# Performance work log

Measured on AMD Instinct MI355X. Metric: run time of the kernel, lower is better.

## Reference

```python
import jax, jax.numpy as jnp
import numpy as np

N_NODES = 100000
N_EDGES = 3200000
F_IN = 256
D_OUT = 64
BATCH = 4096
N_FIELDS = 20


def setup_inputs() -> dict:
    key = jax.random.key(0)
    k1, k2, k3, k4 = jax.random.split(key, 4)
    features = jax.random.normal(k1, (N_NODES, F_IN), dtype=jnp.float32)
    edge_index = jax.random.randint(k2, (2, N_EDGES), 0, N_NODES, dtype=jnp.int32)
    W = jax.random.normal(k3, (F_IN, D_OUT), dtype=jnp.float32) * 0.05
    b = jnp.zeros((D_OUT,), dtype=jnp.float32)
    x = jax.random.randint(k4, (BATCH, N_FIELDS), 0, N_NODES, dtype=jnp.int32)
    return {"features": features, "edge_index": edge_index, "W": W, "b": b, "x": x}


def reference(features, edge_index, W, b, x):
    # PyG GCNConv: add self-loops, symmetric normalization, linear transform,
    # scatter-add aggregation, then final index by x.
    n = features.shape[0]
    loop = jnp.arange(n, dtype=edge_index.dtype)
    src = jnp.concatenate([edge_index[0], loop])  # [E+N]
    dst = jnp.concatenate([edge_index[1], loop])
    ones = jnp.ones(src.shape[0], dtype=features.dtype)
    deg = jax.ops.segment_sum(ones, dst, num_segments=n)  # in-degree incl. self-loop
    deg_inv_sqrt = jnp.where(deg > 0, jax.lax.rsqrt(deg), 0.0)
    norm = deg_inv_sqrt[src] * deg_inv_sqrt[dst]  # [E+N]
    xw = features @ W  # [N, D] -- transform before aggregation (fewer FLOPs)
    msg = xw[src] * norm[:, None]  # gather + scale
    out = jax.ops.segment_sum(msg, dst, num_segments=n) + b  # [N, D]
    return out[x]  # [batch, num_fields, D]
```

## Files before the change

### kernel.cpp

```cpp
#include <hip/hip_runtime.h>
#include <hip/hip_bf16.h>

#define N_NODES 100000
#define N_EDGES 3200000
#define F_IN 256
#define D_OUT 64
#define BATCH 4096
#define N_FIELDS 20
#define N_ENTRIES (BATCH * N_FIELDS)

#define NBUCKET 512
#define NPB 196
#define N_PAD (NBUCKET * NPB)
#define EPB 8192
#define NBLK ((N_EDGES + EPB - 1) / EPB)
#define BUCKET_CAP 8192
#define SCAN_B 512
#define NSB (N_PAD / SCAN_B)

typedef short bf16x8 __attribute__((ext_vector_type(8)));
typedef float f32x4 __attribute__((ext_vector_type(4)));

static __device__ __forceinline__ float bfbits2f(unsigned short u) {
    return __uint_as_float((unsigned)u << 16);
}
static __device__ __forceinline__ unsigned short f2bf_bits(float x) {
    __hip_bfloat16 h = __float2bfloat16(x);
    return *reinterpret_cast<unsigned short*>(&h);
}

__global__ __launch_bounds__(256) void k_hist(const uint4* __restrict__ dst4,
                                              unsigned short* __restrict__ perBlockCnt) {
    __shared__ unsigned hist[NBUCKET];
    hist[threadIdx.x] = 0;
    hist[threadIdx.x + 256] = 0;
    __syncthreads();
    int base4 = blockIdx.x * (EPB / 4);
#pragma unroll
    for (int k = 0; k < EPB / 1024; k++) {
        int e4 = base4 + k * 256 + threadIdx.x;
        if (e4 < N_EDGES / 4) {
            uint4 d = dst4[e4];
            atomicAdd(&hist[d.x / NPB], 1u);
            atomicAdd(&hist[d.y / NPB], 1u);
            atomicAdd(&hist[d.z / NPB], 1u);
            atomicAdd(&hist[d.w / NPB], 1u);
        }
    }
    __syncthreads();
    perBlockCnt[(threadIdx.x) * NBLK + blockIdx.x] = (unsigned short)hist[threadIdx.x];
    perBlockCnt[(threadIdx.x + 256) * NBLK + blockIdx.x] = (unsigned short)hist[threadIdx.x + 256];
}

__global__ __launch_bounds__(256) void k_colscan_w(unsigned short* __restrict__ perBlockCnt,
                                                   int* __restrict__ bucketTot) {
    int gw = (blockIdx.x * 256 + threadIdx.x) >> 6;
    int lane = threadIdx.x & 63;
    if (gw >= NBUCKET) return;
    unsigned running = 0;
    for (int c = 0; c < (NBLK + 63) / 64; c++) {
        int blk = c * 64 + lane;
        int idx = gw * NBLK + blk;
        unsigned v = (blk < NBLK) ? perBlockCnt[idx] : 0;
        unsigned orig = v;
#pragma unroll
        for (int d = 1; d < 64; d <<= 1) {
            unsigned t = __shfl_up(v, d, 64);
            if (lane >= d) v += t;
        }
        if (blk < NBLK) perBlockCnt[idx] = (unsigned short)(running + v - orig);
        running += __shfl(v, 63, 64);
    }
    if (lane == 0) bucketTot[gw] = (int)running;
}

__global__ __launch_bounds__(512) void k_basescan(const int* __restrict__ bucketTot,
                                                  int* __restrict__ bucketBase) {
    __shared__ int sh[NBUCKET];
    int tid = threadIdx.x;
    int v = bucketTot[tid];
    sh[tid] = v;
    __syncthreads();
    for (int off = 1; off < NBUCKET; off <<= 1) {
        int t = (tid >= off) ? sh[tid - off] : 0;
        __syncthreads();
        sh[tid] += t;
        __syncthreads();
    }
    bucketBase[tid] = sh[tid] - v;
    if (tid == NBUCKET - 1) bucketBase[NBUCKET] = sh[NBUCKET - 1];
}

__global__ __launch_bounds__(256) void k_bucket_scatter(const uint4* __restrict__ src4,
                                                        const uint4* __restrict__ dst4,
                                                        const int* __restrict__ bucketBase,
                                                        const unsigned short* __restrict__ perBlockCnt,
                                                        unsigned* __restrict__ bucketData) {
    __shared__ unsigned slotBase[NBUCKET];
    slotBase[threadIdx.x] = (unsigned)bucketBase[threadIdx.x] +
                            (unsigned)perBlockCnt[threadIdx.x * NBLK + blockIdx.x];
    slotBase[threadIdx.x + 256] = (unsigned)bucketBase[threadIdx.x + 256] +
                                  (unsigned)perBlockCnt[(threadIdx.x + 256) * NBLK + blockIdx.x];
    __syncthreads();
    int base4 = blockIdx.x * (EPB / 4);
#pragma unroll
    for (int k = 0; k < EPB / 1024; k++) {
        int e4 = base4 + k * 256 + threadIdx.x;
        if (e4 < N_EDGES / 4) {
            uint4 s = src4[e4];
            uint4 d = dst4[e4];
            unsigned ss[4] = {s.x, s.y, s.z, s.w};
            unsigned dd[4] = {d.x, d.y, d.z, d.w};
#pragma unroll
            for (int j = 0; j < 4; j++) {
                unsigned b = dd[j] / NPB;
                unsigned ld = dd[j] - b * NPB;
                unsigned slot = atomicAdd(&slotBase[b], 1u);
                bucketData[slot] = ss[j] | (ld << 17);
            }
        }
    }
}

__global__ __launch_bounds__(256) void kx_cnt(const int* __restrict__ x,
                                              int* __restrict__ nodeEntCnt,
                                              unsigned* __restrict__ refBits) {
    int ent = blockIdx.x * blockDim.x + threadIdx.x;
    if (ent < N_ENTRIES) {
        int node = x[ent];
        atomicAdd(&nodeEntCnt[node], 1);
        atomicOr(&refBits[node >> 5], 1u << (node & 31));
    }
}

__global__ __launch_bounds__(512) void kx_scan_local(const int* __restrict__ nodeEntCnt,
                                                     int* __restrict__ localE,
                                                     int* __restrict__ blockSumsE) {
    __shared__ int sh[SCAN_B];
    int g = blockIdx.x * SCAN_B + threadIdx.x;
    int v = (g < N_PAD) ? nodeEntCnt[g] : 0;
    sh[threadIdx.x] = v;
    __syncthreads();
    for (int off = 1; off < SCAN_B; off <<= 1) {
        int t = (threadIdx.x >= off) ? sh[threadIdx.x - off] : 0;
        __syncthreads();
        sh[threadIdx.x] += t;
        __syncthreads();
    }
    int incl = sh[threadIdx.x];
    if (g < N_PAD) localE[g] = incl - v;
    if (threadIdx.x == SCAN_B - 1) blockSumsE[blockIdx.x] = incl;
}

__global__ void kx_scan_blocks(const int* __restrict__ blockSumsE,
                               int* __restrict__ blockBaseE) {
    if (threadIdx.x == 0 && blockIdx.x == 0) {
        int s = 0;
        for (int i = 0; i < NSB; i++) {
            blockBaseE[i] = s;
            s += blockSumsE[i];
        }
    }
}

__global__ __launch_bounds__(256) void kx_scatter(const int* __restrict__ x,
                                                  int* __restrict__ localE,
                                                  const int* __restrict__ blockBaseE,
                                                  int* __restrict__ entGrouped) {
    int ent = blockIdx.x * blockDim.x + threadIdx.x;
    if (ent < N_ENTRIES) {
        int node = x[ent];
        int posL = atomicAdd(&localE[node], 1);
        entGrouped[blockBaseE[node >> 9] + posL] = ent;
    }
}

__global__ __launch_bounds__(256) void k_bucket_csr(unsigned* __restrict__ bucketData,
                                                    const int* __restrict__ bucketBase,
                                                    const unsigned* __restrict__ refBits,
                                                    int* __restrict__ rowStart,
                                                    unsigned short* __restrict__ deg) {
    __shared__ unsigned words[BUCKET_CAP];
    __shared__ unsigned srcsorted[BUCKET_CAP];
    __shared__ unsigned nodeCount[NPB];
    __shared__ unsigned sscan[256];
    __shared__ unsigned cursor[NPB];
    __shared__ unsigned char refF[NPB];

    int b = blockIdx.x;
    int base = bucketBase[b];
    int cnt = bucketBase[b + 1] - base;
    if (cnt > BUCKET_CAP) cnt = BUCKET_CAP;
    int tid = threadIdx.x;

    for (int j = tid; j < NPB; j += 256) nodeCount[j] = 0;
    __syncthreads();

    for (int i = tid; i < cnt; i += 256) {
        unsigned w = bucketData[base + i];
        words[i] = w;
        atomicAdd(&nodeCount[w >> 17], 1u);
    }
    __syncthreads();

    int firstNode = b * NPB;
    unsigned refCnt = 0;
    if (tid < NPB) {
        int node = firstNode + tid;
        unsigned isRef = (refBits[node >> 5] >> (node & 31)) & 1u;
        refF[tid] = (unsigned char)isRef;
        refCnt = isRef ? nodeCount[tid] : 0;
        deg[node] = (unsigned short)nodeCount[tid];
    }
    sscan[tid] = refCnt;
    __syncthreads();
    for (int off = 1; off < 256; off <<= 1) {
        unsigned t = (tid >= off) ? sscan[tid - off] : 0;
        __syncthreads();
        sscan[tid] += t;
        __syncthreads();
    }

    if (tid < NPB) {
        unsigned excl = sscan[tid] - refCnt;
        rowStart[firstNode + tid] = base + (int)excl;
        cursor[tid] = excl;
    }
    __syncthreads();

    for (int i = tid; i < cnt; i += 256) {
        unsigned w = words[i];
        unsigned ld = w >> 17;
        if (refF[ld]) {
            unsigned slot = atomicAdd(&cursor[ld], 1u);
            srcsorted[slot] = w & 0x1FFFFu;
        }
    }
    __syncthreads();

    int refTotal = (int)sscan[255];
    for (int i = tid; i < refTotal; i += 256)
        bucketData[base + i] = srcsorted[i];
}

__global__ void k_wtconv(const float* __restrict__ W, unsigned short* __restrict__ WTbf) {
    int i = blockIdx.x * blockDim.x + threadIdx.x;
    if (i >= D_OUT * F_IN) return;
    int n = i >> 8, k = i & 255;
    WTbf[i] = f2bf_bits(W[k * D_OUT + n]);
}

__global__ __launch_bounds__(256) void k_gemm_mfma(const float* __restrict__ feat,
                                                   const unsigned short* __restrict__ WTbf,
                                                   const unsigned short* __restrict__ deg,
                                                   unsigned short* __restrict__ y) {
    __shared__ unsigned short wt[64 * 264];
    int tid = threadIdx.x;
    {
        int r = tid >> 2, seg = tid & 3;
        const uint4* gsrc = (const uint4*)(WTbf + r * 256 + seg * 64);
        uint4* ldst = (uint4*)&wt[r * 264 + seg * 64];
#pragma unroll
        for (int q = 0; q < 8; q++) ldst[q] = gsrc[q];
    }
    __syncthreads();

    int wave = tid >> 6, lane = tid & 63;
    int quad = lane >> 4, m = lane & 15;
    int rowT = blockIdx.x * 64 + wave * 16;
    int row = rowT + m;
    int rowC = (row < N_NODES) ? row : (N_NODES - 1);
    const float* fb = feat + (size_t)rowC * F_IN + quad * 8;

    f32x4 acc0 = {0.f, 0.f, 0.f, 0.f};
    f32x4 acc1 = acc0, acc2 = acc0, acc3 = acc0;

#pragma unroll
    for (int kk = 0; kk < 8; kk++) {
        float4 x0 = *(const float4*)(fb + kk * 32);
        float4 x1 = *(const float4*)(fb + kk * 32 + 4);
        bf16x8 a;
        a[0] = (short)f2bf_bits(x0.x); a[1] = (short)f2bf_bits(x0.y);
        a[2] = (short)f2bf_bits(x0.z); a[3] = (short)f2bf_bits(x0.w);
        a[4] = (short)f2bf_bits(x1.x); a[5] = (short)f2bf_bits(x1.y);
        a[6] = (short)f2bf_bits(x1.z); a[7] = (short)f2bf_bits(x1.w);
        int kbase = kk * 32 + quad * 8;
        bf16x8 b0 = *(const bf16x8*)&wt[(0 * 16 + m) * 264 + kbase];
        bf16x8 b1 = *(const bf16x8*)&wt[(1 * 16 + m) * 264 + kbase];
        bf16x8 b2 = *(const bf16x8*)&wt[(2 * 16 + m) * 264 + kbase];
        bf16x8 b3 = *(const bf16x8*)&wt[(3 * 16 + m) * 264 + kbase];
        acc0 = __builtin_amdgcn_mfma_f32_16x16x32_bf16(a, b0, acc0, 0, 0, 0);
        acc1 = __builtin_amdgcn_mfma_f32_16x16x32_bf16(a, b1, acc1, 0, 0, 0);
        acc2 = __builtin_amdgcn_mfma_f32_16x16x32_bf16(a, b2, acc2, 0, 0, 0);
        acc3 = __builtin_amdgcn_mfma_f32_16x16x32_bf16(a, b3, acc3, 0, 0, 0);
    }

    float dv[4];
#pragma unroll
    for (int r = 0; r < 4; r++) {
        int rr = rowT + quad * 4 + r;
        dv[r] = rsqrtf((float)(deg[rr] + 1));
    }
#pragma unroll
    for (int r = 0; r < 4; r++) {
        int rr = rowT + quad * 4 + r;
        if (rr < N_NODES) {
            size_t o = (size_t)rr * D_OUT + m;
            y[o]      = f2bf_bits(acc0[r] * dv[r]);
            y[o + 16] = f2bf_bits(acc1[r] * dv[r]);
            y[o + 32] = f2bf_bits(acc2[r] * dv[r]);
            y[o + 48] = f2bf_bits(acc3[r] * dv[r]);
        }
    }
}

__global__ __launch_bounds__(256) void k_agg(const int* __restrict__ entGrouped,
                                             const int* __restrict__ localE,
                                             const int* __restrict__ blockBaseE,
                                             const int* __restrict__ rowStart,
                                             const unsigned short* __restrict__ deg,
                                             const unsigned* __restrict__ sortedSrc,
                                             const unsigned short* __restrict__ y,
                                             const float* __restrict__ b,
                                             float* __restrict__ out) {
    int g = blockIdx.x * blockDim.x + threadIdx.x;
    int i = g >> 6, lane = g & 63;
    if (i >= N_PAD) return;
    int gEnd = blockBaseE[i >> 9] + localE[i];
    int gStart = (i == 0) ? 0 : (blockBaseE[(i - 1) >> 9] + localE[i - 1]);
    int cntEnt = gEnd - gStart;
    if (cntEnt <= 0) return;

    int start = rowStart[i];
    int cnt = deg[i];
    float disI = rsqrtf((float)(cnt + 1));
    float self = bfbits2f(y[(size_t)i * D_OUT + lane]);
    float s0 = 0.f, s1 = 0.f, s2 = 0.f, s3 = 0.f;
    float s4 = 0.f, s5 = 0.f, s6 = 0.f, s7 = 0.f;
    int e = 0;
    for (; e + 8 <= cnt; e += 8) {
        unsigned i0 = sortedSrc[start + e];
        unsigned i1 = sortedSrc[start + e + 1];
        unsigned i2 = sortedSrc[start + e + 2];
        unsigned i3 = sortedSrc[start + e + 3];
        unsigned i4 = sortedSrc[start + e + 4];
        unsigned i5 = sortedSrc[start + e + 5];
        unsigned i6 = sortedSrc[start + e + 6];
        unsigned i7 = sortedSrc[start + e + 7];
        s0 += bfbits2f(y[(size_t)i0 * D_OUT + lane]);
        s1 += bfbits2f(y[(size_t)i1 * D_OUT + lane]);
        s2 += bfbits2f(y[(size_t)i2 * D_OUT + lane]);
        s3 += bfbits2f(y[(size_t)i3 * D_OUT + lane]);
        s4 += bfbits2f(y[(size_t)i4 * D_OUT + lane]);
        s5 += bfbits2f(y[(size_t)i5 * D_OUT + lane]);
        s6 += bfbits2f(y[(size_t)i6 * D_OUT + lane]);
        s7 += bfbits2f(y[(size_t)i7 * D_OUT + lane]);
    }
    for (; e + 2 <= cnt; e += 2) {
        unsigned i0 = sortedSrc[start + e];
        unsigned i1 = sortedSrc[start + e + 1];
        s0 += bfbits2f(y[(size_t)i0 * D_OUT + lane]);
        s1 += bfbits2f(y[(size_t)i1 * D_OUT + lane]);
    }
    if (e < cnt) {
        unsigned i0 = sortedSrc[start + e];
        s0 += bfbits2f(y[(size_t)i0 * D_OUT + lane]);
    }
    float sum = self + (((s0 + s1) + (s2 + s3)) + ((s4 + s5) + (s6 + s7)));
    float val = disI * sum + b[lane];
    for (int j = 0; j < cntEnt; j++) {
        int ent = entGrouped[gStart + j];
        out[(size_t)ent * D_OUT + lane] = val;
    }
}

extern "C" void kernel_launch(void* const* d_in, const int* in_sizes, int n_in,
                              void* d_out, int out_size, void* d_ws, size_t ws_size,
                              hipStream_t stream) {
    const float* feat     = (const float*)d_in[0];
    const int* edge_index = (const int*)d_in[1];
    const float* W        = (const float*)d_in[2];
    const float* bsrc     = (const float*)d_in[3];
    const int* x          = (const int*)d_in[4];
    float* out            = (float*)d_out;

    const uint4* src4 = (const uint4*)edge_index;
    const uint4* dst4 = (const uint4*)(edge_index + N_EDGES);

    char* ws = (char*)d_ws;
    size_t off = 0;
    auto alloc = [&](size_t bytes) {
        size_t o = off;
        off = (off + bytes + 255) & ~(size_t)255;
        return o;
    };
    int* bucketBase = (int*)(ws + alloc((size_t)(NBUCKET + 1) * 4));
    int* bucketTot  = (int*)(ws + alloc((size_t)NBUCKET * 4));
    size_t pcOff = alloc((size_t)N_PAD * 4);
    unsigned short* perBlockCnt = (unsigned short*)(ws + pcOff);
    int* nodeEntCnt = (int*)(ws + pcOff);
    int* entGrouped = (int*)(ws + pcOff);
    unsigned* refBits = (unsigned*)(ws + alloc((size_t)(N_PAD / 8)));
    int* rowStart   = (int*)(ws + alloc((size_t)N_PAD * 4));
    unsigned short* deg = (unsigned short*)(ws + alloc((size_t)N_PAD * 2));
    unsigned short* WTbf = (unsigned short*)(ws + alloc((size_t)D_OUT * F_IN * 2));
    int* localE     = (int*)(ws + alloc((size_t)N_PAD * 4));
    int* blockSumsE = (int*)(ws + alloc((size_t)NSB * 4));
    int* blockBaseE = (int*)(ws + alloc((size_t)NSB * 4));
    unsigned* bucketData = (unsigned*)(ws + alloc((size_t)N_EDGES * 4));
    unsigned short* y = (unsigned short*)(ws + alloc((size_t)N_NODES * D_OUT * 2));
    (void)ws_size; (void)in_sizes; (void)n_in; (void)out_size;

    const int T = 256;
    k_hist<<<NBLK, T, 0, stream>>>(dst4, perBlockCnt);
    k_colscan_w<<<(NBUCKET * 64 + T - 1) / T, T, 0, stream>>>(perBlockCnt, bucketTot);
    k_basescan<<<1, NBUCKET, 0, stream>>>(bucketTot, bucketBase);
    k_bucket_scatter<<<NBLK, T, 0, stream>>>(src4, dst4, bucketBase, perBlockCnt, bucketData);
    hipMemsetAsync(nodeEntCnt, 0, (size_t)N_PAD * 4, stream);
    hipMemsetAsync(refBits, 0, (size_t)(N_PAD / 8), stream);
    kx_cnt<<<(N_ENTRIES + T - 1) / T, T, 0, stream>>>(x, nodeEntCnt, refBits);
    kx_scan_local<<<NSB, SCAN_B, 0, stream>>>(nodeEntCnt, localE, blockSumsE);
    kx_scan_blocks<<<1, 64, 0, stream>>>(blockSumsE, blockBaseE);
    kx_scatter<<<(N_ENTRIES + T - 1) / T, T, 0, stream>>>(x, localE, blockBaseE, entGrouped);
    k_bucket_csr<<<NBUCKET, T, 0, stream>>>(bucketData, bucketBase, refBits, rowStart, deg);
    k_wtconv<<<(D_OUT * F_IN + T - 1) / T, T, 0, stream>>>(W, WTbf);
    k_gemm_mfma<<<(N_NODES + 63) / 64, T, 0, stream>>>(feat, WTbf, deg, y);
    k_agg<<<((size_t)N_PAD * 64 + T - 1) / T, T, 0, stream>>>(
        entGrouped, localE, blockBaseE, rowStart, deg, bucketData, y, bsrc, out);
}
```

Measured before the change: 341.6 us.

## Gather bf16 pairs per lane and split neighbors across wave halves in aggregation

```diff
diff --git a/kernel.cpp b/kernel.cpp
--- a/kernel.cpp
+++ b/kernel.cpp
@@ -320,7 +320,7 @@
                                              const int* __restrict__ rowStart,
                                              const unsigned short* __restrict__ deg,
                                              const unsigned* __restrict__ sortedSrc,
-                                             const unsigned short* __restrict__ y,
+                                             const unsigned* __restrict__ y32,
                                              const float* __restrict__ b,
                                              float* __restrict__ out) {
     int g = blockIdx.x * blockDim.x + threadIdx.x;
@@ -331,46 +331,45 @@
     int cntEnt = gEnd - gStart;
     if (cntEnt <= 0) return;
 
+    int half = lane >> 5, l = lane & 31;
     int start = rowStart[i];
     int cnt = deg[i];
     float disI = rsqrtf((float)(cnt + 1));
-    float self = bfbits2f(y[(size_t)i * D_OUT + lane]);
-    float s0 = 0.f, s1 = 0.f, s2 = 0.f, s3 = 0.f;
-    float s4 = 0.f, s5 = 0.f, s6 = 0.f, s7 = 0.f;
-    int e = 0;
-    for (; e + 8 <= cnt; e += 8) {
-        unsigned i0 = sortedSrc[start + e];
-        unsigned i1 = sortedSrc[start + e + 1];
-        unsigned i2 = sortedSrc[start + e + 2];
-        unsigned i3 = sortedSrc[start + e + 3];
-        unsigned i4 = sortedSrc[start + e + 4];
-        unsigned i5 = sortedSrc[start + e + 5];
-        unsigned i6 = sortedSrc[start + e + 6];
-        unsigned i7 = sortedSrc[start + e + 7];
-        s0 += bfbits2f(y[(size_t)i0 * D_OUT + lane]);
-        s1 += bfbits2f(y[(size_t)i1 * D_OUT + lane]);
-        s2 += bfbits2f(y[(size_t)i2 * D_OUT + lane]);
-        s3 += bfbits2f(y[(size_t)i3 * D_OUT + lane]);
-        s4 += bfbits2f(y[(size_t)i4 * D_OUT + lane]);
-        s5 += bfbits2f(y[(size_t)i5 * D_OUT + lane]);
-        s6 += bfbits2f(y[(size_t)i6 * D_OUT + lane]);
-        s7 += bfbits2f(y[(size_t)i7 * D_OUT + lane]);
-    }
-    for (; e + 2 <= cnt; e += 2) {
-        unsigned i0 = sortedSrc[start + e];
-        unsigned i1 = sortedSrc[start + e + 1];
-        s0 += bfbits2f(y[(size_t)i0 * D_OUT + lane]);
-        s1 += bfbits2f(y[(size_t)i1 * D_OUT + lane]);
-    }
-    if (e < cnt) {
-        unsigned i0 = sortedSrc[start + e];
-        s0 += bfbits2f(y[(size_t)i0 * D_OUT + lane]);
-    }
-    float sum = self + (((s0 + s1) + (s2 + s3)) + ((s4 + s5) + (s6 + s7)));
-    float val = disI * sum + b[lane];
-    for (int j = 0; j < cntEnt; j++) {
+
+    float a0 = 0.f, a1 = 0.f;
+    if (half == 0) {
+        unsigned sv = y32[(size_t)i * 32 + l];
+        a0 = __uint_as_float(sv << 16);
+        a1 = __uint_as_float(sv & 0xffff0000u);
+    }
+
+    for (int ebase = 0; ebase < cnt; ebase += 64) {
+        int limit = cnt - ebase;
+        if (limit > 64) limit = 64;
+        unsigned eidx = 0;
+        if (lane < limit) eidx = sortedSrc[start + ebase + lane];
+#pragma unroll 4
+        for (int j = 0; j < limit; j += 2) {
+            unsigned r0 = __shfl(eidx, j, 64);
+            bool pair = (j + 1 < limit);
+            unsigned r1 = __shfl(eidx, pair ? (j + 1) : j, 64);
+            unsigned r = half ? r1 : r0;
+            unsigned v = y32[(size_t)r * 32 + l];
+            if (half == 0 || pair) {
+                a0 += __uint_as_float(v << 16);
+                a1 += __uint_as_float(v & 0xffff0000u);
+            }
+        }
+    }
+
+    a0 += __shfl_xor(a0, 32, 64);
+    a1 += __shfl_xor(a1, 32, 64);
+
+    float2 bl = ((const float2*)b)[l];
+    float2 val = make_float2(disI * a0 + bl.x, disI * a1 + bl.y);
+    for (int j = half; j < cntEnt; j += 2) {
         int ent = entGrouped[gStart + j];
-        out[(size_t)ent * D_OUT + lane] = val;
+        ((float2*)out)[(size_t)ent * 32 + l] = val;
     }
 }
 
@@ -416,8 +415,7 @@
     k_colscan_w<<<(NBUCKET * 64 + T - 1) / T, T, 0, stream>>>(perBlockCnt, bucketTot);
     k_basescan<<<1, NBUCKET, 0, stream>>>(bucketTot, bucketBase);
     k_bucket_scatter<<<NBLK, T, 0, stream>>>(src4, dst4, bucketBase, perBlockCnt, bucketData);
-    hipMemsetAsync(nodeEntCnt, 0, (size_t)N_PAD * 4, stream);
-    hipMemsetAsync(refBits, 0, (size_t)(N_PAD / 8), stream);
+    hipMemsetAsync(nodeEntCnt, 0, (size_t)N_PAD * 4 + (size_t)(N_PAD / 8), stream);
     kx_cnt<<<(N_ENTRIES + T - 1) / T, T, 0, stream>>>(x, nodeEntCnt, refBits);
     kx_scan_local<<<NSB, SCAN_B, 0, stream>>>(nodeEntCnt, localE, blockSumsE);
     kx_scan_blocks<<<1, 64, 0, stream>>>(blockSumsE, blockBaseE);
@@ -426,5 +424,6 @@
     k_wtconv<<<(D_OUT * F_IN + T - 1) / T, T, 0, stream>>>(W, WTbf);
     k_gemm_mfma<<<(N_NODES + 63) / 64, T, 0, stream>>>(feat, WTbf, deg, y);
     k_agg<<<((size_t)N_PAD * 64 + T - 1) / T, T, 0, stream>>>(
-        entGrouped, localE, blockBaseE, rowStart, deg, bucketData, y, bsrc, out);
-}
+        entGrouped, localE, blockBaseE, rowStart, deg, bucketData,
+        (const unsigned*)y, bsrc, out);
+}
```

Result: slower. 368.1 us (+7.8%).
